# Kernel tuning notes

Measured on AMD Instinct MI355X. Metric: run time of the kernel, lower is better.

Reference implementation:

```python
import jax, jax.numpy as jnp
import numpy as np

N, E, FT_IN, HID, FT_OUT, H = 32768, 524288, 256, 256, 512, 4
C = HID // H  # per-head dim = 64


def gatv2_conv(x, edge_index, w_l, b_l, w_r, b_r, att, bias):
    """PyG GATv2Conv (eval mode, add_self_loops=True, concat=True)."""
    n = x.shape[0]
    loop = jnp.arange(n)
    src = jnp.concatenate([edge_index[0], loop])  # j (source / neighbor)
    dst = jnp.concatenate([edge_index[1], loop])  # i (target)
    x_l = (x @ w_l + b_l).reshape(n, H, C)
    x_r = (x @ w_r + b_r).reshape(n, H, C)
    e = jax.nn.leaky_relu(x_l[src] + x_r[dst], 0.2)        # [E+N, H, C]
    logits = jnp.einsum('ehc,hc->eh', e, att)              # [E+N, H]
    m = jax.ops.segment_max(logits, dst, num_segments=n)
    m = jnp.where(jnp.isfinite(m), m, 0.0)
    p = jnp.exp(logits - m[dst])
    s = jax.ops.segment_sum(p, dst, num_segments=n)
    alpha = p / (s[dst] + 1e-16)                           # scatter-softmax over in-edges
    out = jax.ops.segment_sum(alpha[:, :, None] * x_l[src], dst, num_segments=n)
    return out.reshape(n, H * C) + bias


def gelu(x):
    return jax.nn.gelu(x, approximate=False)  # torch nn.GELU default (erf)


def setup_inputs() -> dict:
    key = jax.random.key(0)
    ks = jax.random.split(key, 24)
    sc = lambda fan_in: 1.0 / np.sqrt(fan_in)
    d = {
        'x': jax.random.normal(ks[0], (N, FT_IN), jnp.float32),
        'edge_index': jax.random.randint(ks[1], (2, E), 0, N, dtype=jnp.int32),
        'batch': jnp.repeat(jnp.arange(64, dtype=jnp.int32), N // 64),
        'batch_size': 64,
        # conv1 params
        'w1_l': jax.random.normal(ks[2], (FT_IN, HID), jnp.float32) * sc(FT_IN),
        'b1_l': jnp.zeros((HID,), jnp.float32),
        'w1_r': jax.random.normal(ks[3], (FT_IN, HID), jnp.float32) * sc(FT_IN),
        'b1_r': jnp.zeros((HID,), jnp.float32),
        'att1': jax.random.normal(ks[4], (H, C), jnp.float32) * sc(C),
        'bias1': jnp.zeros((HID,), jnp.float32),
        # conv2 params
        'w2_l': jax.random.normal(ks[5], (HID, HID), jnp.float32) * sc(HID),
        'b2_l': jnp.zeros((HID,), jnp.float32),
        'w2_r': jax.random.normal(ks[6], (HID, HID), jnp.float32) * sc(HID),
        'b2_r': jnp.zeros((HID,), jnp.float32),
        'att2': jax.random.normal(ks[7], (H, C), jnp.float32) * sc(C),
        'bias2': jnp.zeros((HID,), jnp.float32),
        # MLP head
        'lin1_w': jax.random.normal(ks[8], (HID, 4 * HID), jnp.float32) * sc(HID),
        'lin1_b': jnp.zeros((4 * HID,), jnp.float32),
        'lin2_w': jax.random.normal(ks[9], (4 * HID, HID), jnp.float32) * sc(4 * HID),
        'lin2_b': jnp.zeros((HID,), jnp.float32),
        'fin_w': jax.random.normal(ks[10], (HID, FT_OUT), jnp.float32) * sc(HID),
        'fin_b': jnp.zeros((FT_OUT,), jnp.float32),
    }
    return d


def reference(x, edge_index, batch, batch_size,
              w1_l, b1_l, w1_r, b1_r, att1, bias1,
              w2_l, b2_l, w2_r, b2_r, att2, bias2,
              lin1_w, lin1_b, lin2_w, lin2_b, fin_w, fin_b):
    h = gatv2_conv(x, edge_index, w1_l, b1_l, w1_r, b1_r, att1, bias1)
    h = gelu(h)
    h = gatv2_conv(h, edge_index, w2_l, b2_l, w2_r, b2_r, att2, bias2)
    # global mean pool per graph
    n_graphs = batch_size
    sums = jax.ops.segment_sum(h, batch, num_segments=n_graphs)
    cnts = jax.ops.segment_sum(jnp.ones((h.shape[0],), h.dtype), batch, num_segments=n_graphs)
    graph_mean = sums / jnp.maximum(cnts, 1.0)[:, None]
    # take node 0 of each graph (dropouts are identity in eval)
    z = h.reshape(batch_size, -1, HID)[:, 0, :]
    z = gelu(z @ lin1_w + lin1_b) @ lin2_w + lin2_b
    z = z @ fin_w + fin_b
    return z, graph_mean
```

## Files before the change

### kernel.cpp

```cpp
#include <hip/hip_runtime.h>
#include <hip/hip_bf16.h>
#include <stdint.h>

typedef __attribute__((ext_vector_type(8))) short short8;
typedef __attribute__((ext_vector_type(4))) short short4v;
typedef __attribute__((ext_vector_type(4))) float floatx4;
typedef __attribute__((ext_vector_type(2))) float floatx2;
typedef __hip_bfloat16 bf16;

__device__ __forceinline__ float b2f(bf16 v) { return __bfloat162float(v); }
__device__ __forceinline__ bf16 f2b(float v) { return __float2bfloat16(v); }
__device__ __forceinline__ float gelu_f(float v) {
    return 0.5f * v * (1.0f + erff(v * 0.70710678118654752f));
}
__device__ __forceinline__ floatx2 cvt2(unsigned v) {
    floatx2 r;
    r.x = __uint_as_float(v << 16);
    r.y = __uint_as_float(v & 0xffff0000u);
    return r;
}
template <int CTRL>
__device__ __forceinline__ float dpp_add(float v) {
    int x = __builtin_amdgcn_update_dpp(0, __float_as_int(v), CTRL, 0xf, 0xf, true);
    return v + __int_as_float(x);
}

#define GLD_LDS16(gptr, lptr) \
  __builtin_amdgcn_global_load_lds((const __attribute__((address_space(1))) void*)(gptr), \
                                   (__attribute__((address_space(3))) void*)(lptr), 16, 0, 0)


__global__ void k_count_tr(const int* __restrict__ dst, int* __restrict__ cnt, int E,
                           const float* __restrict__ Wl1, const float* __restrict__ Wr1,
                           const float* __restrict__ Wl2, const float* __restrict__ Wr2,
                           bf16* __restrict__ Wt,
                           const float* __restrict__ x, bf16* __restrict__ xb) {
    int bx = blockIdx.x;
    if (bx < 512) {
        int g = bx * 256 + threadIdx.x;
        if (g * 4 < E) {
            int4 d = ((const int4*)dst)[g];
            atomicAdd(&cnt[d.x], 1);
            atomicAdd(&cnt[d.y], 1);
            atomicAdd(&cnt[d.z], 1);
            atomicAdd(&cnt[d.w], 1);
        }
    } else if (bx < 1536) {
        int b = bx - 512;
        int r = b & 255, half = (b >> 8) & 1, layer = b >> 9;
        int c = threadIdx.x;
        const float* W = layer ? (half ? Wr2 : Wl2) : (half ? Wr1 : Wl1);
        Wt[(size_t)(layer * 512 + half * 256 + c) * 256 + r] = f2b(W[r * 256 + c]);
    } else {
        int b = bx - 1536;
        size_t base = ((size_t)b * 256 + threadIdx.x) * 32;
        const float4* xin = (const float4*)(x + base);
        #pragma unroll
        for (int q = 0; q < 4; q++) {
            float4 a = xin[2 * q];
            float4 c = xin[2 * q + 1];
            bf16 t[8] = {f2b(a.x), f2b(a.y), f2b(a.z), f2b(a.w),
                         f2b(c.x), f2b(c.y), f2b(c.z), f2b(c.w)};
            *(short8*)(xb + base + q * 8) = *(const short8*)t;
        }
    }
}

__global__ __launch_bounds__(1024) void k_scan(const int* __restrict__ cnt,
                                               int* __restrict__ row_ptr,
                                               int* __restrict__ fill, int n) {
    __shared__ int sdata[1024];
    int t = threadIdx.x;
    int base = t * 32;
    int local[32];
    const int4* c4 = (const int4*)(cnt + base);
    int vals[32];
    #pragma unroll
    for (int q = 0; q < 8; q++) {
        int4 v = c4[q];
        vals[q * 4 + 0] = v.x; vals[q * 4 + 1] = v.y;
        vals[q * 4 + 2] = v.z; vals[q * 4 + 3] = v.w;
    }
    int sum = 0;
    #pragma unroll
    for (int k = 0; k < 32; k++) { local[k] = sum; sum += vals[k]; }
    sdata[t] = sum;
    __syncthreads();
    for (int off = 1; off < 1024; off <<= 1) {
        int v = (t >= off) ? sdata[t - off] : 0;
        __syncthreads();
        sdata[t] += v;
        __syncthreads();
    }
    int excl = sdata[t] - sum;
    #pragma unroll
    for (int k = 0; k < 32; k++) {
        int v = excl + local[k];
        row_ptr[base + k] = v;
        fill[base + k] = v;
    }
    if (t == 1023) row_ptr[n] = excl + sum;
}

__device__ __forceinline__ void gemm_body(const bf16* __restrict__ A,
                                          const bf16* __restrict__ Bt,
                                          const float* __restrict__ biasL,
                                          const float* __restrict__ biasR,
                                          bf16* __restrict__ C,
                                          int K, int m0, int n0,
                                          bf16* __restrict__ smem) {
    bf16* As = smem;
    bf16* Bs = smem + 8192;
    const int tid  = threadIdx.x;
    const int wave = tid >> 6;
    const int lane = tid & 63;
    const int quad = lane >> 4;
    const int l16  = lane & 15;
    const int wm = (wave & 1) * 64;
    const int wn = (wave >> 1) * 64;
    const int scole = ((lane & 7) ^ (lane >> 3)) * 8;
    const int srow  = lane >> 3;

    floatx4 acc[4][4] = {};

    for (int k0 = 0; k0 < K; k0 += 64) {
        #pragma unroll
        for (int i = 0; i < 4; i++) {
            int chunk = i * 4 + wave;
            int row = chunk * 8 + srow;
            GLD_LDS16(A + (size_t)(m0 + row) * K + k0 + scole,
                      (char*)As + chunk * 1024 + lane * 16);
            GLD_LDS16(Bt + (size_t)(n0 + row) * K + k0 + scole,
                      (char*)Bs + chunk * 1024 + lane * 16);
        }
        __syncthreads();
        #pragma unroll
        for (int ks = 0; ks < 2; ks++) {
            short8 af[4], bfr[4];
            int pk = ((ks * 4 + quad) ^ (l16 & 7)) * 8;
            #pragma unroll
            for (int i = 0; i < 4; i++) {
                af[i]  = *(const short8*)&As[(wm + i * 16 + l16) * 64 + pk];
                bfr[i] = *(const short8*)&Bs[(wn + i * 16 + l16) * 64 + pk];
            }
            #pragma unroll
            for (int i = 0; i < 4; i++)
                #pragma unroll
                for (int j = 0; j < 4; j++)
                    acc[i][j] = __builtin_amdgcn_mfma_f32_16x16x32_bf16(af[i], bfr[j], acc[i][j], 0, 0, 0);
        }
        __syncthreads();
    }

    float bvj[4];
    #pragma unroll
    for (int j = 0; j < 4; j++) {
        int gcol = n0 + wn + j * 16 + l16;
        bvj[j] = (gcol < 256) ? biasL[gcol] : biasR[gcol - 256];
    }
    #pragma unroll
    for (int h = 0; h < 2; h++) {
        if ((wave & 1) == h) {
            #pragma unroll
            for (int j = 0; j < 4; j++) {
                int lcol = wn + j * 16 + l16;
                #pragma unroll
                for (int i = 0; i < 4; i++)
                    #pragma unroll
                    for (int r = 0; r < 4; r++)
                        smem[(i * 16 + quad * 4 + r) * 136 + lcol] = f2b(acc[i][j][r] + bvj[j]);
            }
        }
        __syncthreads();
        {
            int rl = tid >> 4;
            int cs = (tid & 15) * 8;
            #pragma unroll
            for (int p = 0; p < 4; p++) {
                int row = p * 16 + rl;
                short8 v = *(const short8*)&smem[row * 136 + cs];
                *(short8*)(C + (size_t)(m0 + h * 64 + row) * 512 + n0 + cs) = v;
            }
        }
        if (h == 0) __syncthreads();
    }
}

__global__ __launch_bounds__(256) void k_scatter_gemm(const int* __restrict__ src,
                                                      const int* __restrict__ dst,
                                                      int* __restrict__ fill,
                                                      int* __restrict__ col, int E,
                                                      const bf16* __restrict__ A,
                                                      const bf16* __restrict__ Bt,
                                                      const float* __restrict__ biasL,
                                                      const float* __restrict__ biasR,
                                                      bf16* __restrict__ C, int K) {
    __shared__ bf16 smem[16384];
    int bx = blockIdx.x;
    int rem = bx % 3;
    if (rem == 2) {
        int g = (bx / 3) * 256 + threadIdx.x;
        if (g * 4 < E) {
            int4 d = ((const int4*)dst)[g];
            int4 sv = ((const int4*)src)[g];
            int p;
            p = atomicAdd(&fill[d.x], 1); col[p] = sv.x;
            p = atomicAdd(&fill[d.y], 1); col[p] = sv.y;
            p = atomicAdd(&fill[d.z], 1); col[p] = sv.z;
            p = atomicAdd(&fill[d.w], 1); col[p] = sv.w;
        }
    } else {
        int gid = (bx / 3) * 2 + rem;
        int n0 = (gid & 3) * 128;
        int m0 = (gid >> 2) * 128;
        gemm_body(A, Bt, biasL, biasR, C, K, m0, n0, smem);
    }
}

__global__ __launch_bounds__(256) void k_gemm2(const bf16* __restrict__ A,
                                               const bf16* __restrict__ Bt,
                                               const float* __restrict__ biasL,
                                               const float* __restrict__ biasR,
                                               bf16* __restrict__ C, int K) {
    __shared__ bf16 smem[16384];
    int n0 = blockIdx.x * 128;
    int m0 = blockIdx.y * 128;
    gemm_body(A, Bt, biasL, biasR, C, K, m0, n0, smem);
}

__global__ __launch_bounds__(128) void k_agg(const bf16* __restrict__ xlr,
                                             const float* __restrict__ att,
                                             const int* __restrict__ row_ptr,
                                             const int* __restrict__ col,
                                             const float* __restrict__ bias,
                                             bf16* __restrict__ out, int do_gelu) {
    int wave = threadIdx.x >> 6, lane = threadIdx.x & 63;
    int i = blockIdx.x * 2 + wave;
    int hl = lane & 31;
    int half = lane >> 5;
    unsigned f = (hl >> 3) * 64 + (hl & 7) * 8;

    floatx2 att6v[4], att4v[4], xrv[4];
    {
        floatx4 a0 = *(const floatx4*)(att + f);
        floatx4 a1 = *(const floatx4*)(att + f + 4);
        att6v[0] = (floatx2){0.6f * a0[0], 0.6f * a0[1]};
        att6v[1] = (floatx2){0.6f * a0[2], 0.6f * a0[3]};
        att6v[2] = (floatx2){0.6f * a1[0], 0.6f * a1[1]};
        att6v[3] = (floatx2){0.6f * a1[2], 0.6f * a1[3]};
        att4v[0] = (floatx2){0.4f * a0[0], 0.4f * a0[1]};
        att4v[1] = (floatx2){0.4f * a0[2], 0.4f * a0[3]};
        att4v[2] = (floatx2){0.4f * a1[0], 0.4f * a1[1]};
        att4v[3] = (floatx2){0.4f * a1[2], 0.4f * a1[3]};
        unsigned raw[4];
        *(uint4*)raw = *(const uint4*)(xlr + ((unsigned)i * 512u + 256u + f));
        #pragma unroll
        for (int k = 0; k < 4; k++) xrv[k] = cvt2(raw[k]);
    }

    int e0 = row_ptr[i], e1 = row_ptr[i + 1];
    int total = 1 + (e1 - e0);

    int src_c = i;
    if (half == 1 && total > 1) src_c = col[e0];
    unsigned g_cur[4];
    *(uint4*)g_cur = *(const uint4*)(xlr + ((unsigned)src_c * 512u + f));
    int t1 = 2 + half;
    int src_n = (t1 < total) ? col[e0 + t1 - 1] : i;

    float s = 0.f;
    floatx2 acc2[4] = {};

    for (int base = 0; base < total; base += 2) {
        unsigned g_nxt[4];
        *(uint4*)g_nxt = *(const uint4*)(xlr + ((unsigned)src_n * 512u + f));
        int t2 = base + 4 + half;
        int src_n2 = (t2 < total) ? col[e0 + t2 - 1] : i;
        bool valid = (base + half) < total;
        floatx2 xv[4], l2a = {0.f, 0.f}, l2b = {0.f, 0.f};
        #pragma unroll
        for (int k = 0; k < 4; k++) {
            xv[k] = cvt2(g_cur[k]);
            floatx2 u = xv[k] + xrv[k];
            floatx2 au = __builtin_elementwise_abs(u);
            l2a += u * att6v[k];
            l2b += au * att4v[k];
        }
        float l = (l2a.x + l2b.x) + (l2a.y + l2b.y);
        l = dpp_add<0xB1>(l);
        l = dpp_add<0x4E>(l);
        l = dpp_add<0x141>(l);
        float p = valid ? __expf(l) : 0.f;
        s += p;
        floatx2 p2 = {p, p};
        #pragma unroll
        for (int k = 0; k < 4; k++) acc2[k] += p2 * xv[k];
        #pragma unroll
        for (int k = 0; k < 4; k++) g_cur[k] = g_nxt[k];
        src_n = src_n2;
    }

    s += __shfl_xor(s, 32, 64);
    #pragma unroll
    for (int k = 0; k < 4; k++) {
        acc2[k].x += __shfl_xor(acc2[k].x, 32, 64);
        acc2[k].y += __shfl_xor(acc2[k].y, 32, 64);
    }

    if (half == 0) {
        float inv = 1.0f / (s + 1e-16f);
        bf16 ov[8];
        #pragma unroll
        for (int k = 0; k < 4; k++) {
            float v0 = acc2[k].x * inv + bias[f + 2 * k];
            float v1 = acc2[k].y * inv + bias[f + 2 * k + 1];
            if (do_gelu) { v0 = gelu_f(v0); v1 = gelu_f(v1); }
            ov[2 * k]     = f2b(v0);
            ov[2 * k + 1] = f2b(v1);
        }
        *(short8*)(out + ((unsigned)i * 256u + f)) = *(const short8*)ov;
    }
}

__device__ __forceinline__ void head_body(const bf16* __restrict__ inB,
                                          const float* __restrict__ inF,
                                          const float* __restrict__ W,
                                          const float* __restrict__ bias,
                                          float* __restrict__ out,
                                          int K, int N, long long row_stride, int act,
                                          int g, int chunk, float* zin, float* red) {
    int t = threadIdx.x;
    int nc = t & 63;
    int kq = t >> 6;
    int n = chunk * 64 + nc;
    for (int k = t; k < K; k += 256)
        zin[k] = inB ? b2f(inB[(size_t)g * row_stride + k])
                     : inF[(size_t)g * row_stride + k];
    __syncthreads();
    const int klen = K >> 2;
    const int kb = kq * klen;
    float acc = 0.f;
    #pragma unroll 8
    for (int k = 0; k < klen; k++)
        acc = fmaf(zin[kb + k], W[(size_t)(kb + k) * N + n], acc);
    red[t] = acc;
    __syncthreads();
    if (kq == 0) {
        float v = red[nc] + red[nc + 64] + red[nc + 128] + red[nc + 192] + bias[n];
        if (act) v = gelu_f(v);
        out[(size_t)g * N + n] = v;
    }
}

__global__ __launch_bounds__(256) void k_pe1(const bf16* __restrict__ hb,
                                             float* __restrict__ part,
                                             const float* __restrict__ lin1w,
                                             const float* __restrict__ lin1b,
                                             float* __restrict__ t1, int PG) {
    __shared__ float zin[256];
    __shared__ float red[256];
    int bx = blockIdx.x;
    if (bx < 512) {
        int g = bx >> 3, p = bx & 7, c = threadIdx.x;
        int rows_per = PG / 8;
        const bf16* base = hb + ((size_t)g * PG + (size_t)p * rows_per) * 256;
        float acc = 0.f;
        for (int r = 0; r < rows_per; r++) acc += b2f(base[(size_t)r * 256 + c]);
        part[((size_t)g * 8 + p) * 256 + c] = acc;
    } else {
        int b = bx - 512;
        head_body(hb, nullptr, lin1w, lin1b, t1, 256, 1024,
                  (long long)PG * 256, 1, b >> 4, b & 15, zin, red);
    }
}

__global__ __launch_bounds__(256) void k_pe2(const float* __restrict__ part,
                                             float* __restrict__ outPool, int PG,
                                             const float* __restrict__ t1,
                                             const float* __restrict__ lin2w,
                                             const float* __restrict__ lin2b,
                                             float* __restrict__ t2) {
    __shared__ float zin[1024];
    __shared__ float red[256];
    int bx = blockIdx.x;
    if (bx < 64) {
        int g = bx, c = threadIdx.x;
        float acc = 0.f;
        for (int p = 0; p < 8; p++) acc += part[((size_t)g * 8 + p) * 256 + c];
        outPool[g * 256 + c] = acc / (float)PG;
    } else {
        int b = bx - 64;
        head_body(nullptr, t1, lin2w, lin2b, t2, 1024, 256,
                  1024, 0, b >> 2, b & 3, zin, red);
    }
}

__global__ __launch_bounds__(256) void k_fin(const float* __restrict__ t2,
                                             const float* __restrict__ finw,
                                             const float* __restrict__ finb,
                                             float* __restrict__ out) {
    __shared__ float zin[256];
    __shared__ float red[256];
    head_body(nullptr, t2, finw, finb, out, 256, 512,
              256, 0, blockIdx.x, blockIdx.y, zin, red);
}

extern "C" void kernel_launch(void* const* d_in, const int* in_sizes, int n_in,
                              void* d_out, int out_size, void* d_ws, size_t ws_size,
                              hipStream_t stream) {
    const float* x     = (const float*)d_in[0];
    const int*   ei    = (const int*)d_in[1];
    const float* w1_l  = (const float*)d_in[4];
    const float* b1_l  = (const float*)d_in[5];
    const float* w1_r  = (const float*)d_in[6];
    const float* b1_r  = (const float*)d_in[7];
    const float* att1  = (const float*)d_in[8];
    const float* bias1 = (const float*)d_in[9];
    const float* w2_l  = (const float*)d_in[10];
    const float* b2_l  = (const float*)d_in[11];
    const float* w2_r  = (const float*)d_in[12];
    const float* b2_r  = (const float*)d_in[13];
    const float* att2  = (const float*)d_in[14];
    const float* bias2 = (const float*)d_in[15];
    const float* lin1w = (const float*)d_in[16];
    const float* lin1b = (const float*)d_in[17];
    const float* lin2w = (const float*)d_in[18];
    const float* lin2b = (const float*)d_in[19];
    const float* finw  = (const float*)d_in[20];
    const float* finb  = (const float*)d_in[21];

    const int N  = in_sizes[0] / 256;
    const int E  = in_sizes[1] / 2;
    const int NG = 64;
    const int PG = N / NG;

    char* ws = (char*)d_ws;
    size_t off = 0;
    bf16* xlr = (bf16*)(ws + off); off += (size_t)N * 512 * 2;
    bf16* hb  = (bf16*)(ws + off); off += (size_t)N * 256 * 2;
    bf16* wt  = (bf16*)(ws + off); off += 2 * 512 * 256 * 2;
    int* row_ptr = (int*)(ws + off); off += (size_t)(N + 4) * 4;
    int* cnt     = (int*)(ws + off); off += (size_t)N * 4;
    int* fill    = (int*)(ws + off); off += (size_t)N * 4;
    int* col     = (int*)(ws + off); off += (size_t)E * 4;
    float* pws   = (float*)(ws + off); off += (size_t)NG * 8 * 256 * 4;
    float* t1    = (float*)(ws + off); off += (size_t)NG * 1024 * 4;
    float* t2    = (float*)(ws + off); off += (size_t)NG * 256 * 4;

    bf16* xb = hb;

    const int* srcv = ei;
    const int* dstv = ei + E;

    hipMemsetAsync(cnt, 0, (size_t)N * 4, stream);
    k_count_tr<<<512 + 1024 + 1024, 256, 0, stream>>>(dstv, cnt, E,
                                                      w1_l, w1_r, w2_l, w2_r, wt, x, xb);
    k_scan<<<1, 1024, 0, stream>>>(cnt, row_ptr, fill, N);

    k_scatter_gemm<<<512 + 1024, 256, 0, stream>>>(srcv, dstv, fill, col, E,
                                                   xb, wt, b1_l, b1_r, xlr, 256);
    k_agg<<<N / 2, 128, 0, stream>>>(xlr, att1, row_ptr, col, bias1, hb, 1);

    dim3 gg(4, N / 128);
    k_gemm2<<<gg, 256, 0, stream>>>(hb, wt + 512 * 256, b2_l, b2_r, xlr, 256);
    k_agg<<<N / 2, 128, 0, stream>>>(xlr, att2, row_ptr, col, bias2, hb, 0);

    float* outp = (float*)d_out;
    k_pe1<<<512 + 1024, 256, 0, stream>>>(hb, pws, lin1w, lin1b, t1, PG);
    k_pe2<<<64 + 256, 256, 0, stream>>>(pws, outp + 64 * 512, PG, t1, lin2w, lin2b, t2);
    dim3 gf(NG, 512 / 64);
    k_fin<<<gf, 256, 0, stream>>>(t2, finw, finb, outp);
}
```

Before: 334.4 us.

## Record edge ranks during counting and widen aggregation to 16 features per lane

The counting pass now keeps the atomicAdd return value as a per-edge rank, so the CSR fill writes col[row_ptr[d]+rank] directly instead of issuing a second round of atomics on a fill array. The aggregation kernel is reorganised so each lane handles 16 features and a wave processes four neighbour edges at once instead of two. This uses fewer DPP reduction steps per edge and gives more loads in flight, at the cost of more registers and an extra cross-lane shuffle stage at the end. An E-sized rank buffer is added to the workspace.

```diff
diff --git a/kernel.cpp b/kernel.cpp
--- a/kernel.cpp
+++ b/kernel.cpp
@@ -34,16 +34,19 @@
                            const float* __restrict__ Wl1, const float* __restrict__ Wr1,
                            const float* __restrict__ Wl2, const float* __restrict__ Wr2,
                            bf16* __restrict__ Wt,
-                           const float* __restrict__ x, bf16* __restrict__ xb) {
+                           const float* __restrict__ x, bf16* __restrict__ xb,
+                           int* __restrict__ rank) {
     int bx = blockIdx.x;
     if (bx < 512) {
         int g = bx * 256 + threadIdx.x;
         if (g * 4 < E) {
             int4 d = ((const int4*)dst)[g];
-            atomicAdd(&cnt[d.x], 1);
-            atomicAdd(&cnt[d.y], 1);
-            atomicAdd(&cnt[d.z], 1);
-            atomicAdd(&cnt[d.w], 1);
+            int4 rk;
+            rk.x = atomicAdd(&cnt[d.x], 1);
+            rk.y = atomicAdd(&cnt[d.y], 1);
+            rk.z = atomicAdd(&cnt[d.z], 1);
+            rk.w = atomicAdd(&cnt[d.w], 1);
+            ((int4*)rank)[g] = rk;
         }
     } else if (bx < 1536) {
         int b = bx - 512;
@@ -67,8 +70,7 @@
 }
 
 __global__ __launch_bounds__(1024) void k_scan(const int* __restrict__ cnt,
-                                               int* __restrict__ row_ptr,
-                                               int* __restrict__ fill, int n) {
+                                               int* __restrict__ row_ptr, int n) {
     __shared__ int sdata[1024];
     int t = threadIdx.x;
     int base = t * 32;
@@ -94,11 +96,8 @@
     }
     int excl = sdata[t] - sum;
     #pragma unroll
-    for (int k = 0; k < 32; k++) {
-        int v = excl + local[k];
-        row_ptr[base + k] = v;
-        fill[base + k] = v;
-    }
+    for (int k = 0; k < 32; k++)
+        row_ptr[base + k] = excl + local[k];
     if (t == 1023) row_ptr[n] = excl + sum;
 }
 
@@ -188,7 +187,8 @@
 
 __global__ __launch_bounds__(256) void k_scatter_gemm(const int* __restrict__ src,
                                                       const int* __restrict__ dst,
-                                                      int* __restrict__ fill,
+                                                      const int* __restrict__ row_ptr,
+                                                      const int* __restrict__ rank,
                                                       int* __restrict__ col, int E,
                                                       const bf16* __restrict__ A,
                                                       const bf16* __restrict__ Bt,
@@ -203,11 +203,11 @@
         if (g * 4 < E) {
             int4 d = ((const int4*)dst)[g];
             int4 sv = ((const int4*)src)[g];
-            int p;
-            p = atomicAdd(&fill[d.x], 1); col[p] = sv.x;
-            p = atomicAdd(&fill[d.y], 1); col[p] = sv.y;
-            p = atomicAdd(&fill[d.z], 1); col[p] = sv.z;
-            p = atomicAdd(&fill[d.w], 1); col[p] = sv.w;
+            int4 rk = ((const int4*)rank)[g];
+            col[row_ptr[d.x] + rk.x] = sv.x;
+            col[row_ptr[d.y] + rk.y] = sv.y;
+            col[row_ptr[d.z] + rk.z] = sv.z;
+            col[row_ptr[d.w] + rk.w] = sv.w;
         }
     } else {
         int gid = (bx / 3) * 2 + rem;
@@ -236,50 +236,49 @@
                                              bf16* __restrict__ out, int do_gelu) {
     int wave = threadIdx.x >> 6, lane = threadIdx.x & 63;
     int i = blockIdx.x * 2 + wave;
-    int hl = lane & 31;
-    int half = lane >> 5;
-    unsigned f = (hl >> 3) * 64 + (hl & 7) * 8;
-
-    floatx2 att6v[4], att4v[4], xrv[4];
+    int q = lane >> 4;
+    int r = lane & 15;
+    unsigned f = (unsigned)(r >> 2) * 64 + (unsigned)(r & 3) * 16;
+
+    floatx2 att6v[8], att4v[8], xrv[8];
+    #pragma unroll
+    for (int k = 0; k < 4; k++) {
+        floatx4 a = *(const floatx4*)(att + f + 4 * k);
+        att6v[2 * k]     = (floatx2){0.6f * a[0], 0.6f * a[1]};
+        att6v[2 * k + 1] = (floatx2){0.6f * a[2], 0.6f * a[3]};
+        att4v[2 * k]     = (floatx2){0.4f * a[0], 0.4f * a[1]};
+        att4v[2 * k + 1] = (floatx2){0.4f * a[2], 0.4f * a[3]};
+    }
     {
-        floatx4 a0 = *(const floatx4*)(att + f);
-        floatx4 a1 = *(const floatx4*)(att + f + 4);
-        att6v[0] = (floatx2){0.6f * a0[0], 0.6f * a0[1]};
-        att6v[1] = (floatx2){0.6f * a0[2], 0.6f * a0[3]};
-        att6v[2] = (floatx2){0.6f * a1[0], 0.6f * a1[1]};
-        att6v[3] = (floatx2){0.6f * a1[2], 0.6f * a1[3]};
-        att4v[0] = (floatx2){0.4f * a0[0], 0.4f * a0[1]};
-        att4v[1] = (floatx2){0.4f * a0[2], 0.4f * a0[3]};
-        att4v[2] = (floatx2){0.4f * a1[0], 0.4f * a1[1]};
-        att4v[3] = (floatx2){0.4f * a1[2], 0.4f * a1[3]};
-        unsigned raw[4];
-        *(uint4*)raw = *(const uint4*)(xlr + ((unsigned)i * 512u + 256u + f));
-        #pragma unroll
-        for (int k = 0; k < 4; k++) xrv[k] = cvt2(raw[k]);
+        unsigned raw[8];
+        *(uint4*)raw       = *(const uint4*)(xlr + ((unsigned)i * 512u + 256u + f));
+        *(uint4*)(raw + 4) = *(const uint4*)(xlr + ((unsigned)i * 512u + 256u + f + 8));
+        #pragma unroll
+        for (int k = 0; k < 8; k++) xrv[k] = cvt2(raw[k]);
     }
 
     int e0 = row_ptr[i], e1 = row_ptr[i + 1];
     int total = 1 + (e1 - e0);
 
-    int src_c = i;
-    if (half == 1 && total > 1) src_c = col[e0];
-    unsigned g_cur[4];
-    *(uint4*)g_cur = *(const uint4*)(xlr + ((unsigned)src_c * 512u + f));
-    int t1 = 2 + half;
+    int src_c = (q > 0 && q < total) ? col[e0 + q - 1] : i;
+    unsigned g_cur[8], g_nxt[8];
+    *(uint4*)g_cur       = *(const uint4*)(xlr + ((unsigned)src_c * 512u + f));
+    *(uint4*)(g_cur + 4) = *(const uint4*)(xlr + ((unsigned)src_c * 512u + f + 8));
+    int t1 = 4 + q;
     int src_n = (t1 < total) ? col[e0 + t1 - 1] : i;
 
     float s = 0.f;
-    floatx2 acc2[4] = {};
-
-    for (int base = 0; base < total; base += 2) {
-        unsigned g_nxt[4];
-        *(uint4*)g_nxt = *(const uint4*)(xlr + ((unsigned)src_n * 512u + f));
-        int t2 = base + 4 + half;
+    floatx2 acc2[8] = {};
+
+    for (int base = 0; base < total; base += 4) {
+        *(uint4*)g_nxt       = *(const uint4*)(xlr + ((unsigned)src_n * 512u + f));
+        *(uint4*)(g_nxt + 4) = *(const uint4*)(xlr + ((unsigned)src_n * 512u + f + 8));
+        int t2 = base + 8 + q;
         int src_n2 = (t2 < total) ? col[e0 + t2 - 1] : i;
-        bool valid = (base + half) < total;
-        floatx2 xv[4], l2a = {0.f, 0.f}, l2b = {0.f, 0.f};
-        #pragma unroll
-        for (int k = 0; k < 4; k++) {
+        bool valid = (base + q) < total;
+        floatx2 xv[8], l2a = {0.f, 0.f}, l2b = {0.f, 0.f};
+        #pragma unroll
+        for (int k = 0; k < 8; k++) {
             xv[k] = cvt2(g_cur[k]);
             floatx2 u = xv[k] + xrv[k];
             floatx2 au = __builtin_elementwise_abs(u);
@@ -289,36 +288,39 @@
         float l = (l2a.x + l2b.x) + (l2a.y + l2b.y);
         l = dpp_add<0xB1>(l);
         l = dpp_add<0x4E>(l);
-        l = dpp_add<0x141>(l);
         float p = valid ? __expf(l) : 0.f;
         s += p;
         floatx2 p2 = {p, p};
         #pragma unroll
-        for (int k = 0; k < 4; k++) acc2[k] += p2 * xv[k];
-        #pragma unroll
-        for (int k = 0; k < 4; k++) g_cur[k] = g_nxt[k];
+        for (int k = 0; k < 8; k++) acc2[k] += p2 * xv[k];
+        #pragma unroll
+        for (int k = 0; k < 8; k++) g_cur[k] = g_nxt[k];
         src_n = src_n2;
     }
 
+    s += __shfl_xor(s, 16, 64);
     s += __shfl_xor(s, 32, 64);
     #pragma unroll
-    for (int k = 0; k < 4; k++) {
+    for (int k = 0; k < 8; k++) {
+        acc2[k].x += __shfl_xor(acc2[k].x, 16, 64);
         acc2[k].x += __shfl_xor(acc2[k].x, 32, 64);
+        acc2[k].y += __shfl_xor(acc2[k].y, 16, 64);
         acc2[k].y += __shfl_xor(acc2[k].y, 32, 64);
     }
 
-    if (half == 0) {
+    if (q == 0) {
         float inv = 1.0f / (s + 1e-16f);
-        bf16 ov[8];
-        #pragma unroll
-        for (int k = 0; k < 4; k++) {
+        bf16 ov[16];
+        #pragma unroll
+        for (int k = 0; k < 8; k++) {
             float v0 = acc2[k].x * inv + bias[f + 2 * k];
             float v1 = acc2[k].y * inv + bias[f + 2 * k + 1];
             if (do_gelu) { v0 = gelu_f(v0); v1 = gelu_f(v1); }
             ov[2 * k]     = f2b(v0);
             ov[2 * k + 1] = f2b(v1);
         }
-        *(short8*)(out + ((unsigned)i * 256u + f)) = *(const short8*)ov;
+        *(short8*)(out + ((unsigned)i * 256u + f))     = *(const short8*)ov;
+        *(short8*)(out + ((unsigned)i * 256u + f + 8)) = *(const short8*)(ov + 8);
     }
 }
 
@@ -441,8 +443,8 @@
     bf16* wt  = (bf16*)(ws + off); off += 2 * 512 * 256 * 2;
     int* row_ptr = (int*)(ws + off); off += (size_t)(N + 4) * 4;
     int* cnt     = (int*)(ws + off); off += (size_t)N * 4;
-    int* fill    = (int*)(ws + off); off += (size_t)N * 4;
     int* col     = (int*)(ws + off); off += (size_t)E * 4;
+    int* rank    = (int*)(ws + off); off += (size_t)E * 4;
     float* pws   = (float*)(ws + off); off += (size_t)NG * 8 * 256 * 4;
     float* t1    = (float*)(ws + off); off += (size_t)NG * 1024 * 4;
     float* t2    = (float*)(ws + off); off += (size_t)NG * 256 * 4;
@@ -454,10 +456,11 @@
 
     hipMemsetAsync(cnt, 0, (size_t)N * 4, stream);
     k_count_tr<<<512 + 1024 + 1024, 256, 0, stream>>>(dstv, cnt, E,
-                                                      w1_l, w1_r, w2_l, w2_r, wt, x, xb);
-    k_scan<<<1, 1024, 0, stream>>>(cnt, row_ptr, fill, N);
-
-    k_scatter_gemm<<<512 + 1024, 256, 0, stream>>>(srcv, dstv, fill, col, E,
+                                                      w1_l, w1_r, w2_l, w2_r, wt, x, xb,
+                                                      rank);
+    k_scan<<<1, 1024, 0, stream>>>(cnt, row_ptr, N);
+
+    k_scatter_gemm<<<512 + 1024, 256, 0, stream>>>(srcv, dstv, row_ptr, rank, col, E,
                                                    xb, wt, b1_l, b1_r, xlr, 256);
     k_agg<<<N / 2, 128, 0, stream>>>(xlr, att1, row_ptr, col, bias1, hb, 1);
 
```

Result: slower. 364.2 us (+8.9%).

## Record edge ranks during counting and simplify leaky-relu/exp in aggregation

Applied to the files above, without the earlier changes.

The counting pass now saves the value returned by each atomic increment as a per-edge rank. The CSR fill step then places each edge at row_ptr plus its rank, so the second round of atomics and the separate fill array go away. In the aggregation kernel, leaky_relu is computed as max(u, 0.2u) with log2(e) folded into the attention weights, and the exponential is done with a raw v_exp_f32. This removes the abs-based split into two accumulators and the extra multiply inside __expf, at the cost of an extra E-sized rank buffer that is written once and read once.

```diff
diff --git a/kernel.cpp b/kernel.cpp
--- a/kernel.cpp
+++ b/kernel.cpp
@@ -34,16 +34,19 @@
                            const float* __restrict__ Wl1, const float* __restrict__ Wr1,
                            const float* __restrict__ Wl2, const float* __restrict__ Wr2,
                            bf16* __restrict__ Wt,
-                           const float* __restrict__ x, bf16* __restrict__ xb) {
+                           const float* __restrict__ x, bf16* __restrict__ xb,
+                           int* __restrict__ rank) {
     int bx = blockIdx.x;
     if (bx < 512) {
         int g = bx * 256 + threadIdx.x;
         if (g * 4 < E) {
             int4 d = ((const int4*)dst)[g];
-            atomicAdd(&cnt[d.x], 1);
-            atomicAdd(&cnt[d.y], 1);
-            atomicAdd(&cnt[d.z], 1);
-            atomicAdd(&cnt[d.w], 1);
+            int4 rk;
+            rk.x = atomicAdd(&cnt[d.x], 1);
+            rk.y = atomicAdd(&cnt[d.y], 1);
+            rk.z = atomicAdd(&cnt[d.z], 1);
+            rk.w = atomicAdd(&cnt[d.w], 1);
+            ((int4*)rank)[g] = rk;
         }
     } else if (bx < 1536) {
         int b = bx - 512;
@@ -67,8 +70,7 @@
 }
 
 __global__ __launch_bounds__(1024) void k_scan(const int* __restrict__ cnt,
-                                               int* __restrict__ row_ptr,
-                                               int* __restrict__ fill, int n) {
+                                               int* __restrict__ row_ptr, int n) {
     __shared__ int sdata[1024];
     int t = threadIdx.x;
     int base = t * 32;
@@ -94,11 +96,8 @@
     }
     int excl = sdata[t] - sum;
     #pragma unroll
-    for (int k = 0; k < 32; k++) {
-        int v = excl + local[k];
-        row_ptr[base + k] = v;
-        fill[base + k] = v;
-    }
+    for (int k = 0; k < 32; k++)
+        row_ptr[base + k] = excl + local[k];
     if (t == 1023) row_ptr[n] = excl + sum;
 }
 
@@ -188,7 +187,8 @@
 
 __global__ __launch_bounds__(256) void k_scatter_gemm(const int* __restrict__ src,
                                                       const int* __restrict__ dst,
-                                                      int* __restrict__ fill,
+                                                      const int* __restrict__ row_ptr,
+                                                      const int* __restrict__ rank,
                                                       int* __restrict__ col, int E,
                                                       const bf16* __restrict__ A,
                                                       const bf16* __restrict__ Bt,
@@ -203,11 +203,11 @@
         if (g * 4 < E) {
             int4 d = ((const int4*)dst)[g];
             int4 sv = ((const int4*)src)[g];
-            int p;
-            p = atomicAdd(&fill[d.x], 1); col[p] = sv.x;
-            p = atomicAdd(&fill[d.y], 1); col[p] = sv.y;
-            p = atomicAdd(&fill[d.z], 1); col[p] = sv.z;
-            p = atomicAdd(&fill[d.w], 1); col[p] = sv.w;
+            int4 rk = ((const int4*)rank)[g];
+            col[row_ptr[d.x] + rk.x] = sv.x;
+            col[row_ptr[d.y] + rk.y] = sv.y;
+            col[row_ptr[d.z] + rk.z] = sv.z;
+            col[row_ptr[d.w] + rk.w] = sv.w;
         }
     } else {
         int gid = (bx / 3) * 2 + rem;
@@ -240,18 +240,16 @@
     int half = lane >> 5;
     unsigned f = (hl >> 3) * 64 + (hl & 7) * 8;
 
-    floatx2 att6v[4], att4v[4], xrv[4];
+    const float LOG2E = 1.4426950408889634f;
+    const floatx2 c02 = {0.2f, 0.2f};
+    floatx2 attv[4], xrv[4];
     {
         floatx4 a0 = *(const floatx4*)(att + f);
         floatx4 a1 = *(const floatx4*)(att + f + 4);
-        att6v[0] = (floatx2){0.6f * a0[0], 0.6f * a0[1]};
-        att6v[1] = (floatx2){0.6f * a0[2], 0.6f * a0[3]};
-        att6v[2] = (floatx2){0.6f * a1[0], 0.6f * a1[1]};
-        att6v[3] = (floatx2){0.6f * a1[2], 0.6f * a1[3]};
-        att4v[0] = (floatx2){0.4f * a0[0], 0.4f * a0[1]};
-        att4v[1] = (floatx2){0.4f * a0[2], 0.4f * a0[3]};
-        att4v[2] = (floatx2){0.4f * a1[0], 0.4f * a1[1]};
-        att4v[3] = (floatx2){0.4f * a1[2], 0.4f * a1[3]};
+        attv[0] = (floatx2){LOG2E * a0[0], LOG2E * a0[1]};
+        attv[1] = (floatx2){LOG2E * a0[2], LOG2E * a0[3]};
+        attv[2] = (floatx2){LOG2E * a1[0], LOG2E * a1[1]};
+        attv[3] = (floatx2){LOG2E * a1[2], LOG2E * a1[3]};
         unsigned raw[4];
         *(uint4*)raw = *(const uint4*)(xlr + ((unsigned)i * 512u + 256u + f));
         #pragma unroll
@@ -277,20 +275,21 @@
         int t2 = base + 4 + half;
         int src_n2 = (t2 < total) ? col[e0 + t2 - 1] : i;
         bool valid = (base + half) < total;
-        floatx2 xv[4], l2a = {0.f, 0.f}, l2b = {0.f, 0.f};
+        floatx2 xv[4], l2 = {0.f, 0.f};
         #pragma unroll
         for (int k = 0; k < 4; k++) {
             xv[k] = cvt2(g_cur[k]);
             floatx2 u = xv[k] + xrv[k];
-            floatx2 au = __builtin_elementwise_abs(u);
-            l2a += u * att6v[k];
-            l2b += au * att4v[k];
-        }
-        float l = (l2a.x + l2b.x) + (l2a.y + l2b.y);
+            floatx2 lr = __builtin_elementwise_max(u, u * c02);
+            l2 += lr * attv[k];
+        }
+        float l = l2.x + l2.y;
         l = dpp_add<0xB1>(l);
         l = dpp_add<0x4E>(l);
         l = dpp_add<0x141>(l);
-        float p = valid ? __expf(l) : 0.f;
+        float p;
+        asm("v_exp_f32 %0, %1" : "=v"(p) : "v"(l));
+        p = valid ? p : 0.f;
         s += p;
         floatx2 p2 = {p, p};
         #pragma unroll
@@ -441,8 +440,8 @@
     bf16* wt  = (bf16*)(ws + off); off += 2 * 512 * 256 * 2;
     int* row_ptr = (int*)(ws + off); off += (size_t)(N + 4) * 4;
     int* cnt     = (int*)(ws + off); off += (size_t)N * 4;
-    int* fill    = (int*)(ws + off); off += (size_t)N * 4;
     int* col     = (int*)(ws + off); off += (size_t)E * 4;
+    int* rank    = (int*)(ws + off); off += (size_t)E * 4;
     float* pws   = (float*)(ws + off); off += (size_t)NG * 8 * 256 * 4;
     float* t1    = (float*)(ws + off); off += (size_t)NG * 1024 * 4;
     float* t2    = (float*)(ws + off); off += (size_t)NG * 256 * 4;
@@ -454,10 +453,11 @@
 
     hipMemsetAsync(cnt, 0, (size_t)N * 4, stream);
     k_count_tr<<<512 + 1024 + 1024, 256, 0, stream>>>(dstv, cnt, E,
-                                                      w1_l, w1_r, w2_l, w2_r, wt, x, xb);
-    k_scan<<<1, 1024, 0, stream>>>(cnt, row_ptr, fill, N);
-
-    k_scatter_gemm<<<512 + 1024, 256, 0, stream>>>(srcv, dstv, fill, col, E,
+                                                      w1_l, w1_r, w2_l, w2_r, wt, x, xb,
+                                                      rank);
+    k_scan<<<1, 1024, 0, stream>>>(cnt, row_ptr, N);
+
+    k_scatter_gemm<<<512 + 1024, 256, 0, stream>>>(srcv, dstv, row_ptr, rank, col, E,
                                                    xb, wt, b1_l, b1_r, xlr, 256);
     k_agg<<<N / 2, 128, 0, stream>>>(xlr, att1, row_ptr, col, bias1, hb, 1);
 
```

Result: faster. 322.8 us (-3.5%).
